# Optimization experiments

Hardware: AMD Instinct MI355X
Metric: run time of the kernel (lower is better)

The kernel has to match this reference:

```python
import jax, jax.numpy as jnp
import numpy as np

VAR_XY = 0.1  # SSD encoding variances
VAR_WH = 0.2


def _iou(truths, priors):
    # truths [G,4], priors [P,4] in corner form (x1,y1,x2,y2) -> [G,P]
    lt = jnp.maximum(truths[:, None, :2], priors[None, :, :2])
    rb = jnp.minimum(truths[:, None, 2:], priors[None, :, 2:])
    wh = jnp.clip(rb - lt, 0.0, None)
    inter = wh[..., 0] * wh[..., 1]
    area_t = (truths[:, 2] - truths[:, 0]) * (truths[:, 3] - truths[:, 1])
    area_p = (priors[:, 2] - priors[:, 0]) * (priors[:, 3] - priors[:, 1])
    return inter / (area_t[:, None] + area_p[None, :] - inter)


def _encode(truths, matched):
    # truths [G,1,4], matched priors [G,k,4], corner form -> SSD offsets [G,k,4]
    p_cxcy = (matched[..., :2] + matched[..., 2:]) * 0.5
    p_wh = matched[..., 2:] - matched[..., :2]
    g_cxcy = (truths[..., :2] + truths[..., 2:]) * 0.5
    g_wh = truths[..., 2:] - truths[..., :2]
    off_xy = (g_cxcy - p_cxcy) / (VAR_XY * p_wh)
    off_wh = jnp.log(g_wh / p_wh) / VAR_WH
    return jnp.concatenate([off_xy, off_wh], axis=-1)


def setup_inputs() -> dict:
    key = jax.random.key(0)
    k1, k2, k3, k4 = jax.random.split(key, 4)
    B, P, G = 16, 32768, 128
    # priors: valid corner-form boxes built from centers + sizes
    p_c = jax.random.uniform(k1, (B, P, 2), minval=0.1, maxval=0.9)
    p_s = jax.random.uniform(k2, (B, P, 2), minval=0.02, maxval=0.3)
    priors = jnp.concatenate([p_c - p_s * 0.5, p_c + p_s * 0.5], axis=-1)
    rpn_rois = jnp.stack([priors, priors], axis=1)  # [B,2,P,4]; channel 1 used
    # GT boxes, valid corner form
    t_c = jax.random.uniform(k3, (B, G, 2), minval=0.1, maxval=0.9)
    t_s = jax.random.uniform(k4, (B, G, 2), minval=0.05, maxval=0.4)
    targets = jnp.concatenate([t_c - t_s * 0.5, t_c + t_s * 0.5], axis=-1)
    return {"rpn_rois": rpn_rois, "targets": targets, "expand_num": 4}


def reference(rpn_rois, targets, expand_num):
    defaults = rpn_rois[:, 1]  # [B,P,4]

    def per_image(truths, priors):
        ious = _iou(truths, priors)                      # [G,P]
        _, idx = jax.lax.top_k(ious, expand_num)         # [G,k] best priors per GT
        matched = priors[idx]                            # [G,k,4]
        off = _encode(truths[:, None, :], matched)       # [G,k,4]
        return off.reshape(-1, 4)                        # [G*k,4]

    return jax.vmap(per_image)(targets, defaults)        # [B, G*k, 4]
```

## Files before the change

### kernel.cpp

```cpp
#include <hip/hip_runtime.h>

#define B 16
#define P 32768
#define NG 128
#define KTOP 4
#define NBX 32
#define NBY 32
#define NBB (NBX * NBY)
#define SUB 16
#define SUBP (P / SUB)
typedef unsigned long long u64;
typedef unsigned int u32;

__device__ __forceinline__ int bkt(float v) {
    int k = (int)((v + 0.08f) * 32.0f);
    return k < 0 ? 0 : (k > 31 ? 31 : k);
}

__device__ __forceinline__ void ceu(u64 &x, u64 &y) {
    u64 a = x, b = y; bool gt = a > b;
    x = gt ? a : b;  y = gt ? b : a;
}
__device__ __forceinline__ void cef(float &x, float &y) {
    float h = fmaxf(x, y), l = fminf(x, y); x = h; y = l;
}

__global__ __launch_bounds__(256)
void k_hist(const float* __restrict__ rois, u32* __restrict__ cnt, u32* __restrict__ whmax)
{
    const int b = blockIdx.x >> 4, sub = blockIdx.x & 15;
    const int tid = threadIdx.x;
    __shared__ u32 h[NBB];
    for (int j = tid; j < NBB; j += 256) h[j] = 0;
    __syncthreads();

    const float4* __restrict__ pv = (const float4*)(rois + ((size_t)(2 * b + 1)) * P * 4);
    float wmax = 0.f, hmax = 0.f;
    #pragma unroll
    for (int it = 0; it < SUBP / 256; ++it) {
        float4 q = pv[sub * SUBP + it * 256 + tid];
        atomicAdd(&h[bkt(q.x) * NBY + bkt(q.y)], 1u);
        wmax = fmaxf(wmax, q.z - q.x);
        hmax = fmaxf(hmax, q.w - q.y);
    }
    __syncthreads();
    for (int j = tid; j < NBB; j += 256) cnt[(size_t)blockIdx.x * NBB + j] = h[j];

    #pragma unroll
    for (int d = 32; d >= 1; d >>= 1) {
        wmax = fmaxf(wmax, __shfl_down(wmax, d, 64));
        hmax = fmaxf(hmax, __shfl_down(hmax, d, 64));
    }
    if ((tid & 63) == 0) {
        atomicMax(&whmax[b * 2 + 0], __float_as_uint(wmax));
        atomicMax(&whmax[b * 2 + 1], __float_as_uint(hmax));
    }
}

__global__ __launch_bounds__(1024)
void k_scan(u32* __restrict__ cnt, u32* __restrict__ off)
{
    const int b = blockIdx.x, j = threadIdx.x;
    const int lane = j & 63, wv = j >> 6;
    u32 c[SUB], s = 0;
    #pragma unroll
    for (int k = 0; k < SUB; ++k) { c[k] = cnt[(size_t)(b * SUB + k) * NBB + j]; s += c[k]; }

    __shared__ u32 wsum[16];
    u32 incl = s;
    #pragma unroll
    for (int d = 1; d < 64; d <<= 1) {
        u32 v = __shfl_up(incl, d, 64);
        if (lane >= d) incl += v;
    }
    if (lane == 63) wsum[wv] = incl;
    __syncthreads();
    if (j < 16) {
        u32 t = wsum[j];
        #pragma unroll
        for (int d = 1; d < 16; d <<= 1) {
            u32 v = __shfl_up(t, d, 64);
            if (lane >= d) t += v;
        }
        wsum[j] = t;
    }
    __syncthreads();
    u32 excl = (wv ? wsum[wv - 1] : 0u) + incl - s;

    u32 run = excl;
    #pragma unroll
    for (int k = 0; k < SUB; ++k) { cnt[(size_t)(b * SUB + k) * NBB + j] = run; run += c[k]; }
    off[b * (NBB + 1) + j] = excl;
    if (j == 0) off[b * (NBB + 1) + NBB] = P;
}

__global__ __launch_bounds__(256)
void k_scat(const float* __restrict__ rois, const u32* __restrict__ cnt,
            float4* __restrict__ sbox, u32* __restrict__ sidx)
{
    const int b = blockIdx.x >> 4, sub = blockIdx.x & 15;
    const int tid = threadIdx.x;
    __shared__ u32 cur[NBB];
    for (int j = tid; j < NBB; j += 256) cur[j] = cnt[(size_t)blockIdx.x * NBB + j];
    __syncthreads();

    const float4* __restrict__ pv = (const float4*)(rois + ((size_t)(2 * b + 1)) * P * 4);
    #pragma unroll
    for (int it = 0; it < SUBP / 256; ++it) {
        int i = sub * SUBP + it * 256 + tid;
        float4 q = pv[i];
        u32 slot = atomicAdd(&cur[bkt(q.x) * NBY + bkt(q.y)], 1u);
        sbox[(size_t)b * P + slot] = q;
        sidx[(size_t)b * P + slot] = (u32)i;
    }
}

__global__ __launch_bounds__(256, 8)
void k_main(const float* __restrict__ rois, const float* __restrict__ targets,
            const float4* __restrict__ sbox, const u32* __restrict__ sidx,
            const u32* __restrict__ off, const u32* __restrict__ whmax,
            float* __restrict__ out)
{
    #pragma clang fp contract(off)

    const int blk = blockIdx.x;
    const int b   = ((blk & 7) << 1) | ((blk >> 3) & 1);
    const int g   = blk >> 4;
    const int tid = threadIdx.x;
    const int lane = tid & 63, wv = tid >> 6;

    const float* tp = targets + ((size_t)(b * NG + g)) * 4;
    const float t0 = tp[0], t1 = tp[1], t2 = tp[2], t3 = tp[3];
    const float areaT = (t2 - t0) * (t3 - t1);
    const float gw = t2 - t0, gh = t3 - t1;

    const float4* __restrict__ boxb = sbox + (size_t)b * P;
    const u32*    __restrict__ idxb = sidx + (size_t)b * P;
    const u32*    __restrict__ offb = off + b * (NBB + 1);

    __shared__ float sf[4][4];
    __shared__ u64   sm[4][4];
    __shared__ int   seg_lo[NBX], seg_hi[NBX];
    __shared__ int   sh_nseg;

    float w0 = -1.f, w1 = -1.f, w2 = -1.f, w3 = -1.f;
    #pragma unroll
    for (int it = 0; it < 4; ++it) {
        float4 q = boxb[(tid + it * 256) * 32];
        float ap = (q.z - q.x) * (q.w - q.y);
        float ltx = fmaxf(t0, q.x), lty = fmaxf(t1, q.y);
        float rbx = fminf(t2, q.z), rby = fminf(t3, q.w);
        float wx = fmaxf(rbx - ltx, 0.0f);
        float wy = fmaxf(rby - lty, 0.0f);
        float inter = wx * wy;
        float iou = inter / ((areaT + ap) - inter);
        float x = iou, h;
        h = fmaxf(w0, x); x = fminf(w0, x); w0 = h;
        h = fmaxf(w1, x); x = fminf(w1, x); w1 = h;
        h = fmaxf(w2, x); x = fminf(w2, x); w2 = h;
        w3 = fmaxf(w3, x);
    }
    #pragma unroll
    for (int d = 32; d >= 1; d >>= 1) {
        float n0 = __shfl_down(w0, d, 64);
        float n1 = __shfl_down(w1, d, 64);
        float n2 = __shfl_down(w2, d, 64);
        float n3 = __shfl_down(w3, d, 64);
        cef(w0, n3); cef(w1, n2); cef(w2, n1); cef(w3, n0);
        cef(w0, w2); cef(w1, w3); cef(w0, w1); cef(w2, w3);
    }
    if (lane == 0) { sf[wv][0] = w0; sf[wv][1] = w1; sf[wv][2] = w2; sf[wv][3] = w3; }
    __syncthreads();

    if (tid == 0) {
        float m0 = -1.f, m1 = -1.f, m2 = -1.f, m3 = -1.f;
        #pragma unroll
        for (int j = 0; j < 16; ++j) {
            float x = sf[j >> 2][j & 3], h;
            h = fmaxf(m0, x); x = fminf(m0, x); m0 = h;
            h = fmaxf(m1, x); x = fminf(m1, x); m1 = h;
            h = fmaxf(m2, x); x = fminf(m2, x); m2 = h;
            m3 = fmaxf(m3, x);
        }
        int nseg = 0;
        if (m3 > 1e-6f) {
            float lb = m3 * 0.999f;
            float wmaxb = __uint_as_float(whmax[b * 2 + 0]);
            float hmaxb = __uint_as_float(whmax[b * 2 + 1]);
            int bxlo = bkt(t0 + lb * gw - wmaxb) - 1; if (bxlo < 0) bxlo = 0;
            int bxhi = bkt(t2 - lb * gw) + 1;          if (bxhi > 31) bxhi = 31;
            int bylo = bkt(t1 + lb * gh - hmaxb) - 1;  if (bylo < 0) bylo = 0;
            int byhi = bkt(t3 - lb * gh) + 1;          if (byhi > 31) byhi = 31;
            for (int bx = bxlo; bx <= bxhi; ++bx) {
                int lo = (int)offb[bx * NBY + bylo];
                int hi = (int)offb[bx * NBY + byhi + 1];
                if (hi > lo) { seg_lo[nseg] = lo; seg_hi[nseg] = hi; ++nseg; }
            }
        }
        if (nseg == 0) { seg_lo[0] = 0; seg_hi[0] = P; nseg = 1; }
        sh_nseg = nseg;
    }
    __syncthreads();
    const int nseg = sh_nseg;

    u64 k0 = 0, k1 = 0, k2 = 0, k3 = 0;
    for (int s = 0; s < nseg; ++s) {
        const int lo = seg_lo[s], hi = seg_hi[s];
        for (int pos = lo + tid; pos < hi; pos += 256) {
            float4 q = boxb[pos];
            u32 oi = idxb[pos];
            float ap = (q.z - q.x) * (q.w - q.y);
            float ltx = fmaxf(t0, q.x), lty = fmaxf(t1, q.y);
            float rbx = fminf(t2, q.z), rby = fminf(t3, q.w);
            float wx = fmaxf(rbx - ltx, 0.0f);
            float wy = fmaxf(rby - lty, 0.0f);
            float inter = wx * wy;
            float iou = inter / ((areaT + ap) - inter);

            u64 x = ((u64)__float_as_uint(iou) << 32) | (u32)(~oi);
            bool g0 = x > k0, g1 = x > k1, g2 = x > k2, g3 = x > k3;
            u64 n3 = g2 ? k2 : (g3 ? x : k3);
            u64 n2 = g1 ? k1 : (g2 ? x : k2);
            u64 n1 = g0 ? k0 : (g1 ? x : k1);
            u64 n0 = g0 ? x  : k0;
            k0 = n0; k1 = n1; k2 = n2; k3 = n3;
        }
    }

    #pragma unroll
    for (int d = 32; d >= 1; d >>= 1) {
        u64 n0 = __shfl_down(k0, d, 64);
        u64 n1 = __shfl_down(k1, d, 64);
        u64 n2 = __shfl_down(k2, d, 64);
        u64 n3 = __shfl_down(k3, d, 64);
        ceu(k0, n3); ceu(k1, n2); ceu(k2, n1); ceu(k3, n0);
        ceu(k0, k2); ceu(k1, k3); ceu(k0, k1); ceu(k2, k3);
    }
    if (lane == 0) { sm[wv][0] = k0; sm[wv][1] = k1; sm[wv][2] = k2; sm[wv][3] = k3; }
    __syncthreads();

    if (tid == 0) {
        u64 f0 = 0, f1 = 0, f2 = 0, f3 = 0;
        #pragma unroll
        for (int j = 0; j < 16; ++j) {
            u64 x = sm[j >> 2][j & 3];
            bool g0 = x > f0, g1 = x > f1, g2 = x > f2, g3 = x > f3;
            u64 n3 = g2 ? f2 : (g3 ? x : f3);
            u64 n2 = g1 ? f1 : (g2 ? x : f2);
            u64 n1 = g0 ? f0 : (g1 ? x : f1);
            u64 n0 = g0 ? x  : f0;
            f0 = n0; f1 = n1; f2 = n2; f3 = n3;
        }
        const float gcx = (t0 + t2) * 0.5f;
        const float gcy = (t1 + t3) * 0.5f;
        const float4* __restrict__ pv =
            (const float4*)(rois + ((size_t)(2 * b + 1)) * P * 4);
        float4* __restrict__ o4 = (float4*)out;

        u64 ks[KTOP] = {f0, f1, f2, f3};
        #pragma unroll
        for (int k = 0; k < KTOP; ++k) {
            int idx = (int)(~(u32)ks[k]) & (P - 1);
            float4 q = pv[idx];
            float pcx = (q.x + q.z) * 0.5f;
            float pcy = (q.y + q.w) * 0.5f;
            float pw  = q.z - q.x;
            float ph  = q.w - q.y;
            float4 r;
            r.x = (gcx - pcx) / (0.1f * pw);
            r.y = (gcy - pcy) / (0.1f * ph);
            r.z = logf(gw / pw) / 0.2f;
            r.w = logf(gh / ph) / 0.2f;
            o4[((size_t)(b * NG + g)) * KTOP + k] = r;
        }
    }
}

extern "C" void kernel_launch(void* const* d_in, const int* in_sizes, int n_in,
                              void* d_out, int out_size, void* d_ws, size_t ws_size,
                              hipStream_t stream) {
    const float* rois    = (const float*)d_in[0];
    const float* targets = (const float*)d_in[1];
    float* out = (float*)d_out;

    char* w = (char*)d_ws;
    float4* sbox  = (float4*)(w);
    u32*    sidx  = (u32*)  (w + (size_t)B * P * 16);
    u32*    cnt   = (u32*)  (w + (size_t)B * P * 20);
    u32*    off   = (u32*)  (w + (size_t)B * P * 20 + (size_t)B * SUB * NBB * 4);
    u32*    whmax = (u32*)  (w + (size_t)B * P * 20 + (size_t)B * SUB * NBB * 4
                               + (size_t)B * (NBB + 1) * 4);

    hipMemsetAsync(whmax, 0, B * 2 * sizeof(u32), stream);
    k_hist<<<dim3(B * SUB), dim3(256),  0, stream>>>(rois, cnt, whmax);
    k_scan<<<dim3(B),       dim3(1024), 0, stream>>>(cnt, off);
    k_scat<<<dim3(B * SUB), dim3(256),  0, stream>>>(rois, cnt, sbox, sidx);
    k_main<<<dim3(B * NG),  dim3(256),  0, stream>>>(rois, targets, sbox, sidx, off, whmax, out);
}
```

Measured before the change: 138.4 us.

## Fuse scan into scatter, drop memset, and refine candidate bins with a sampled bound

The separate scan kernel and memset are removed. Each scatter block now recomputes the per-batch prefix over bins itself, and per-block width/height maxima are written without atomics and reduced later in the main kernel. The main kernel flattens its candidate segments into one cumulative table so threads stride evenly across all segments. When the candidate set exceeds 4096 boxes, it first samples 1024 candidates to raise the IoU lower bound and rebuilds a tighter bin window. This targets launch overhead and the unbalanced, oversized scan in the main kernel, at the cost of redundant scan work per block and an extra sampling pass with a binary search per element.

Measured after the change: 140.8 us. About the same (+1.7%).

```diff
diff --git a/kernel.cpp b/kernel.cpp
--- a/kernel.cpp
+++ b/kernel.cpp
@@ -26,11 +26,12 @@
 }
 
 __global__ __launch_bounds__(256)
-void k_hist(const float* __restrict__ rois, u32* __restrict__ cnt, u32* __restrict__ whmax)
+void k_hist(const float* __restrict__ rois, u32* __restrict__ cnt, float* __restrict__ whm)
 {
     const int b = blockIdx.x >> 4, sub = blockIdx.x & 15;
     const int tid = threadIdx.x;
     __shared__ u32 h[NBB];
+    __shared__ float red[8];
     for (int j = tid; j < NBB; j += 256) h[j] = 0;
     __syncthreads();
 
@@ -43,65 +44,62 @@
         wmax = fmaxf(wmax, q.z - q.x);
         hmax = fmaxf(hmax, q.w - q.y);
     }
-    __syncthreads();
-    for (int j = tid; j < NBB; j += 256) cnt[(size_t)blockIdx.x * NBB + j] = h[j];
-
     #pragma unroll
     for (int d = 32; d >= 1; d >>= 1) {
         wmax = fmaxf(wmax, __shfl_down(wmax, d, 64));
         hmax = fmaxf(hmax, __shfl_down(hmax, d, 64));
     }
-    if ((tid & 63) == 0) {
-        atomicMax(&whmax[b * 2 + 0], __float_as_uint(wmax));
-        atomicMax(&whmax[b * 2 + 1], __float_as_uint(hmax));
-    }
-}
-
-__global__ __launch_bounds__(1024)
-void k_scan(u32* __restrict__ cnt, u32* __restrict__ off)
+    if ((tid & 63) == 0) { red[(tid >> 6) * 2] = wmax; red[(tid >> 6) * 2 + 1] = hmax; }
+    __syncthreads();
+    for (int j = tid; j < NBB; j += 256) cnt[(size_t)blockIdx.x * NBB + j] = h[j];
+    if (tid == 0) {
+        whm[blockIdx.x * 2 + 0] = fmaxf(fmaxf(red[0], red[2]), fmaxf(red[4], red[6]));
+        whm[blockIdx.x * 2 + 1] = fmaxf(fmaxf(red[1], red[3]), fmaxf(red[5], red[7]));
+    }
+}
+
+__global__ __launch_bounds__(256)
+void k_scat(const float* __restrict__ rois, const u32* __restrict__ cnt,
+            float4* __restrict__ sbox, u32* __restrict__ sidx, u32* __restrict__ off)
 {
-    const int b = blockIdx.x, j = threadIdx.x;
-    const int lane = j & 63, wv = j >> 6;
-    u32 c[SUB], s = 0;
-    #pragma unroll
-    for (int k = 0; k < SUB; ++k) { c[k] = cnt[(size_t)(b * SUB + k) * NBB + j]; s += c[k]; }
-
-    __shared__ u32 wsum[16];
-    u32 incl = s;
+    const int b = blockIdx.x >> 4, sub = blockIdx.x & 15;
+    const int tid = threadIdx.x;
+    const int lane = tid & 63, wv = tid >> 6;
+    __shared__ u32 cur[NBB];
+    __shared__ u32 wpart[4];
+
+    u32 bintot[4] = {0, 0, 0, 0};
+    u32 below[4]  = {0, 0, 0, 0};
+    #pragma unroll
+    for (int k = 0; k < SUB; ++k) {
+        #pragma unroll
+        for (int m = 0; m < 4; ++m) {
+            u32 v = cnt[(size_t)(b * SUB + k) * NBB + 4 * tid + m];
+            bintot[m] += v;
+            if (k < sub) below[m] += v;
+        }
+    }
+    u32 s_local = bintot[0] + bintot[1] + bintot[2] + bintot[3];
+    u32 incl = s_local;
     #pragma unroll
     for (int d = 1; d < 64; d <<= 1) {
         u32 v = __shfl_up(incl, d, 64);
         if (lane >= d) incl += v;
     }
-    if (lane == 63) wsum[wv] = incl;
-    __syncthreads();
-    if (j < 16) {
-        u32 t = wsum[j];
-        #pragma unroll
-        for (int d = 1; d < 16; d <<= 1) {
-            u32 v = __shfl_up(t, d, 64);
-            if (lane >= d) t += v;
-        }
-        wsum[j] = t;
-    }
-    __syncthreads();
-    u32 excl = (wv ? wsum[wv - 1] : 0u) + incl - s;
-
-    u32 run = excl;
-    #pragma unroll
-    for (int k = 0; k < SUB; ++k) { cnt[(size_t)(b * SUB + k) * NBB + j] = run; run += c[k]; }
-    off[b * (NBB + 1) + j] = excl;
-    if (j == 0) off[b * (NBB + 1) + NBB] = P;
-}
-
-__global__ __launch_bounds__(256)
-void k_scat(const float* __restrict__ rois, const u32* __restrict__ cnt,
-            float4* __restrict__ sbox, u32* __restrict__ sidx)
-{
-    const int b = blockIdx.x >> 4, sub = blockIdx.x & 15;
-    const int tid = threadIdx.x;
-    __shared__ u32 cur[NBB];
-    for (int j = tid; j < NBB; j += 256) cur[j] = cnt[(size_t)blockIdx.x * NBB + j];
+    if (lane == 63) wpart[wv] = incl;
+    __syncthreads();
+    u32 wbase = 0;
+    #pragma unroll
+    for (int w = 0; w < 4; ++w) if (w < wv) wbase += wpart[w];
+
+    u32 run = wbase + incl - s_local;
+    #pragma unroll
+    for (int m = 0; m < 4; ++m) {
+        cur[4 * tid + m] = run + below[m];
+        if (sub == 0) off[b * (NBB + 1) + 4 * tid + m] = run;
+        run += bintot[m];
+    }
+    if (sub == 0 && tid == 0) off[b * (NBB + 1) + NBB] = P;
     __syncthreads();
 
     const float4* __restrict__ pv = (const float4*)(rois + ((size_t)(2 * b + 1)) * P * 4);
@@ -115,10 +113,31 @@
     }
 }
 
+__device__ __forceinline__ void build_table(float lb, float t0, float t1, float t2, float t3,
+                                            float gw, float gh, float wm, float hm,
+                                            const u32* __restrict__ offb,
+                                            int* seg_lo, int* cum, int& nseg, int& total)
+{
+    nseg = 0; total = 0;
+    if (lb > 1e-6f) {
+        int bxlo = bkt(t0 + lb * gw - wm) - 1; if (bxlo < 0) bxlo = 0;
+        int bxhi = bkt(t2 - lb * gw) + 1;      if (bxhi > 31) bxhi = 31;
+        int bylo = bkt(t1 + lb * gh - hm) - 1; if (bylo < 0) bylo = 0;
+        int byhi = bkt(t3 - lb * gh) + 1;      if (byhi > 31) byhi = 31;
+        for (int bx = bxlo; bx <= bxhi; ++bx) {
+            int lo = (int)offb[bx * NBY + bylo];
+            int hi = (int)offb[bx * NBY + byhi + 1];
+            if (hi > lo) { seg_lo[nseg] = lo; cum[nseg] = total; total += hi - lo; ++nseg; }
+        }
+    }
+    if (nseg == 0) { seg_lo[0] = 0; cum[0] = 0; total = P; nseg = 1; }
+    cum[nseg] = total;
+}
+
 __global__ __launch_bounds__(256, 8)
 void k_main(const float* __restrict__ rois, const float* __restrict__ targets,
             const float4* __restrict__ sbox, const u32* __restrict__ sidx,
-            const u32* __restrict__ off, const u32* __restrict__ whmax,
+            const u32* __restrict__ off, const float* __restrict__ whm,
             float* __restrict__ out)
 {
     #pragma clang fp contract(off)
@@ -140,8 +159,10 @@
 
     __shared__ float sf[4][4];
     __shared__ u64   sm[4][4];
-    __shared__ int   seg_lo[NBX], seg_hi[NBX];
-    __shared__ int   sh_nseg;
+    __shared__ int   seg_lo[NBX + 2];
+    __shared__ int   cum[NBX + 3];
+    __shared__ int   sh_nseg, sh_total;
+    __shared__ float sh_lb, sh_wm, sh_hm;
 
     float w0 = -1.f, w1 = -1.f, w2 = -1.f, w3 = -1.f;
     #pragma unroll
@@ -182,33 +203,34 @@
             h = fmaxf(m2, x); x = fminf(m2, x); m2 = h;
             m3 = fmaxf(m3, x);
         }
-        int nseg = 0;
-        if (m3 > 1e-6f) {
-            float lb = m3 * 0.999f;
-            float wmaxb = __uint_as_float(whmax[b * 2 + 0]);
-            float hmaxb = __uint_as_float(whmax[b * 2 + 1]);
-            int bxlo = bkt(t0 + lb * gw - wmaxb) - 1; if (bxlo < 0) bxlo = 0;
-            int bxhi = bkt(t2 - lb * gw) + 1;          if (bxhi > 31) bxhi = 31;
-            int bylo = bkt(t1 + lb * gh - hmaxb) - 1;  if (bylo < 0) bylo = 0;
-            int byhi = bkt(t3 - lb * gh) + 1;          if (byhi > 31) byhi = 31;
-            for (int bx = bxlo; bx <= bxhi; ++bx) {
-                int lo = (int)offb[bx * NBY + bylo];
-                int hi = (int)offb[bx * NBY + byhi + 1];
-                if (hi > lo) { seg_lo[nseg] = lo; seg_hi[nseg] = hi; ++nseg; }
-            }
-        }
-        if (nseg == 0) { seg_lo[0] = 0; seg_hi[0] = P; nseg = 1; }
-        sh_nseg = nseg;
-    }
-    __syncthreads();
-    const int nseg = sh_nseg;
-
-    u64 k0 = 0, k1 = 0, k2 = 0, k3 = 0;
-    for (int s = 0; s < nseg; ++s) {
-        const int lo = seg_lo[s], hi = seg_hi[s];
-        for (int pos = lo + tid; pos < hi; pos += 256) {
+        float wm = 0.f, hm = 0.f;
+        #pragma unroll
+        for (int k = 0; k < SUB; ++k) {
+            wm = fmaxf(wm, whm[(b * SUB + k) * 2 + 0]);
+            hm = fmaxf(hm, whm[(b * SUB + k) * 2 + 1]);
+        }
+        sh_wm = wm; sh_hm = hm;
+        float lb = m3 * 0.999f;
+        sh_lb = lb;
+        int nseg, total;
+        build_table(lb, t0, t1, t2, t3, gw, gh, wm, hm, offb, seg_lo, cum, nseg, total);
+        sh_nseg = nseg; sh_total = total;
+    }
+    __syncthreads();
+    int nseg = sh_nseg, total = sh_total;
+
+    if (total > 4096) {
+        float u0 = -1.f, u1 = -1.f, u2 = -1.f, u3 = -1.f;
+        const int stride = total >> 10;
+        #pragma unroll
+        for (int it = 0; it < 4; ++it) {
+            int v = (tid + it * 256) * stride + (stride >> 1);
+            int s = 0;
+            #pragma unroll
+            for (int step = 32; step >= 1; step >>= 1)
+                if (s + step < nseg && cum[s + step] <= v) s += step;
+            int pos = seg_lo[s] + (v - cum[s]);
             float4 q = boxb[pos];
-            u32 oi = idxb[pos];
             float ap = (q.z - q.x) * (q.w - q.y);
             float ltx = fmaxf(t0, q.x), lty = fmaxf(t1, q.y);
             float rbx = fminf(t2, q.z), rby = fminf(t3, q.w);
@@ -216,15 +238,70 @@
             float wy = fmaxf(rby - lty, 0.0f);
             float inter = wx * wy;
             float iou = inter / ((areaT + ap) - inter);
-
-            u64 x = ((u64)__float_as_uint(iou) << 32) | (u32)(~oi);
-            bool g0 = x > k0, g1 = x > k1, g2 = x > k2, g3 = x > k3;
-            u64 n3 = g2 ? k2 : (g3 ? x : k3);
-            u64 n2 = g1 ? k1 : (g2 ? x : k2);
-            u64 n1 = g0 ? k0 : (g1 ? x : k1);
-            u64 n0 = g0 ? x  : k0;
-            k0 = n0; k1 = n1; k2 = n2; k3 = n3;
-        }
+            float x = iou, h;
+            h = fmaxf(u0, x); x = fminf(u0, x); u0 = h;
+            h = fmaxf(u1, x); x = fminf(u1, x); u1 = h;
+            h = fmaxf(u2, x); x = fminf(u2, x); u2 = h;
+            u3 = fmaxf(u3, x);
+        }
+        #pragma unroll
+        for (int d = 32; d >= 1; d >>= 1) {
+            float n0 = __shfl_down(u0, d, 64);
+            float n1 = __shfl_down(u1, d, 64);
+            float n2 = __shfl_down(u2, d, 64);
+            float n3 = __shfl_down(u3, d, 64);
+            cef(u0, n3); cef(u1, n2); cef(u2, n1); cef(u3, n0);
+            cef(u0, u2); cef(u1, u3); cef(u0, u1); cef(u2, u3);
+        }
+        __syncthreads();
+        if (lane == 0) { sf[wv][0] = u0; sf[wv][1] = u1; sf[wv][2] = u2; sf[wv][3] = u3; }
+        __syncthreads();
+        if (tid == 0) {
+            float m0 = -1.f, m1 = -1.f, m2 = -1.f, m3 = -1.f;
+            #pragma unroll
+            for (int j = 0; j < 16; ++j) {
+                float x = sf[j >> 2][j & 3], h;
+                h = fmaxf(m0, x); x = fminf(m0, x); m0 = h;
+                h = fmaxf(m1, x); x = fminf(m1, x); m1 = h;
+                h = fmaxf(m2, x); x = fminf(m2, x); m2 = h;
+                m3 = fmaxf(m3, x);
+            }
+            float lb2 = fmaxf(sh_lb, m3 * 0.999f);
+            if (lb2 > sh_lb) {
+                int ns, tt;
+                build_table(lb2, t0, t1, t2, t3, gw, gh, sh_wm, sh_hm, offb, seg_lo, cum, ns, tt);
+                sh_nseg = ns; sh_total = tt;
+            }
+        }
+        __syncthreads();
+        nseg = sh_nseg; total = sh_total;
+    }
+
+    u64 k0 = 0, k1 = 0, k2 = 0, k3 = 0;
+    for (int v = tid; v < total; v += 256) {
+        int s = 0;
+        #pragma unroll
+        for (int step = 32; step >= 1; step >>= 1)
+            if (s + step < nseg && cum[s + step] <= v) s += step;
+        int pos = seg_lo[s] + (v - cum[s]);
+
+        float4 q = boxb[pos];
+        u32 oi = idxb[pos];
+        float ap = (q.z - q.x) * (q.w - q.y);
+        float ltx = fmaxf(t0, q.x), lty = fmaxf(t1, q.y);
+        float rbx = fminf(t2, q.z), rby = fminf(t3, q.w);
+        float wx = fmaxf(rbx - ltx, 0.0f);
+        float wy = fmaxf(rby - lty, 0.0f);
+        float inter = wx * wy;
+        float iou = inter / ((areaT + ap) - inter);
+
+        u64 x = ((u64)__float_as_uint(iou) << 32) | (u32)(~oi);
+        bool g0 = x > k0, g1 = x > k1, g2 = x > k2, g3 = x > k3;
+        u64 n3 = g2 ? k2 : (g3 ? x : k3);
+        u64 n2 = g1 ? k1 : (g2 ? x : k2);
+        u64 n1 = g0 ? k0 : (g1 ? x : k1);
+        u64 n0 = g0 ? x  : k0;
+        k0 = n0; k1 = n1; k2 = n2; k3 = n3;
     }
 
     #pragma unroll
@@ -284,16 +361,13 @@
     float* out = (float*)d_out;
 
     char* w = (char*)d_ws;
-    float4* sbox  = (float4*)(w);
-    u32*    sidx  = (u32*)  (w + (size_t)B * P * 16);
-    u32*    cnt   = (u32*)  (w + (size_t)B * P * 20);
-    u32*    off   = (u32*)  (w + (size_t)B * P * 20 + (size_t)B * SUB * NBB * 4);
-    u32*    whmax = (u32*)  (w + (size_t)B * P * 20 + (size_t)B * SUB * NBB * 4
-                               + (size_t)B * (NBB + 1) * 4);
-
-    hipMemsetAsync(whmax, 0, B * 2 * sizeof(u32), stream);
-    k_hist<<<dim3(B * SUB), dim3(256),  0, stream>>>(rois, cnt, whmax);
-    k_scan<<<dim3(B),       dim3(1024), 0, stream>>>(cnt, off);
-    k_scat<<<dim3(B * SUB), dim3(256),  0, stream>>>(rois, cnt, sbox, sidx);
-    k_main<<<dim3(B * NG),  dim3(256),  0, stream>>>(rois, targets, sbox, sidx, off, whmax, out);
-}
+    float4* sbox = (float4*)(w);
+    u32*    sidx = (u32*)  (w + (size_t)B * P * 16);
+    u32*    cnt  = (u32*)  (w + (size_t)B * P * 20);
+    u32*    off  = (u32*)  (w + (size_t)B * P * 24);
+    float*  whm  = (float*)(w + (size_t)B * P * 24 + 66560);
+
+    k_hist<<<dim3(B * SUB), dim3(256), 0, stream>>>(rois, cnt, whm);
+    k_scat<<<dim3(B * SUB), dim3(256), 0, stream>>>(rois, cnt, sbox, sidx, off);
+    k_main<<<dim3(B * NG),  dim3(256), 0, stream>>>(rois, targets, sbox, sidx, off, whm, out);
+}
```
